# Kernel tuning notes

Measured on AMD Instinct MI355X. Metric: run time of the kernel, lower is better.

## Reference

```python
import jax, jax.numpy as jnp
import numpy as np

N_NODES = 50000
N_EDGES = 1_600_000
F_IN = 128
F_OUT = 8
K_TAPS = 4
AVG_DEG = 32.0


def setup_inputs() -> dict:
    key = jax.random.key(0)
    k1, k2, k3, k4, k5 = jax.random.split(key, 5)
    x = jax.random.normal(k1, (N_NODES, F_IN), dtype=jnp.float32)
    gso_rows = jax.random.randint(k2, (N_EDGES,), 0, N_NODES, dtype=jnp.int32)
    gso_cols = jax.random.randint(k3, (N_EDGES,), 0, N_NODES, dtype=jnp.int32)
    gso_vals = jax.random.uniform(k4, (N_EDGES,), dtype=jnp.float32) / AVG_DEG
    # filterCoeff = randn(outFeat, filter_order) * 0.1 as in torch __init__
    coeff = jax.random.normal(k5, (F_OUT, K_TAPS), dtype=jnp.float32) * 0.1
    return {"x": x, "gso_rows": gso_rows, "gso_cols": gso_cols,
            "gso_vals": gso_vals, "coeff": coeff}


def reference(x, gso_rows, gso_cols, gso_vals, coeff):
    # Faithful to the torch code INCLUDING its carried-over SpMV state:
    # output feature o uses powers S^{1+o(K-1)} .. S^{o(K-1)+K} of x.
    F_out, K = coeff.shape
    N = x.shape[0]
    max_power = F_out * (K - 1) + 1  # highest S power needed

    def spmv(Z):  # S @ Z via edge-list gather + segment_sum scatter
        return jax.ops.segment_sum(gso_vals[:, None] * Z[gso_cols], gso_rows,
                                   num_segments=N)

    def step(Z, _):
        Zn = spmv(Z)
        return Zn, Zn.sum(axis=1)  # sum over in-features done up-front

    # s[p-1, n] = sum_f (S^p x)[n, f], for p = 1..max_power
    _, s = jax.lax.scan(step, x, None, length=max_power)  # (max_power, N)

    # power index (0-based into s) used by output o, tap i: o*(K-1) + i
    idx = jnp.arange(F_out)[:, None] * (K - 1) + jnp.arange(K)[None, :]  # (F_out, K)
    sg = s[idx]  # (F_out, K, N)
    y = jnp.einsum('ok,okn->no', coeff, sg)  # (N, F_out)
    return y
```

## Files before the change

### kernel.cpp

```cpp
#include <hip/hip_runtime.h>
#include <hip/hip_bf16.h>

#define N_NODES 50000
#define N_EDGES 1600000
#define F_IN    128
#define F_OUT   8
#define K_TAPS  4
#define MAX_POWER 25

#define NBLK    256
#define NTHR    512
#define RPB     196
#define CHUNK   4096
#define NPART   391
#define ECAP_G  8192
#define ECAP_L  7168
#define NITER   14
#define CSB     800

#define FSTRIDE 16

__device__ inline int wave_incl_scan(int v, int lane) {
    #pragma unroll
    for (int off = 1; off < 64; off <<= 1) {
        int t = __shfl_up(v, off, 64);
        if (lane >= off) v += t;
    }
    return v;
}

__device__ inline void st_coh(float* p, float v) {
    __hip_atomic_store(p, v, __ATOMIC_RELAXED, __HIP_MEMORY_SCOPE_AGENT);
}
__device__ inline void st_coh_i(int* p, int v) {
    __hip_atomic_store(p, v, __ATOMIC_RELAXED, __HIP_MEMORY_SCOPE_AGENT);
}
__device__ inline int ld_coh_i(const int* p) {
    return __hip_atomic_load((int*)p, __ATOMIC_RELAXED, __HIP_MEMORY_SCOPE_AGENT);
}

__global__ void rowsum_kernel(const float* __restrict__ x,
                              float* __restrict__ u, int n_nodes) {
    int wave_in_block = threadIdx.x >> 6;
    int lane = threadIdx.x & 63;
    int node = blockIdx.x * 4 + wave_in_block;
    if (node >= n_nodes) return;
    const float2* xp = (const float2*)(x + (size_t)node * F_IN);
    float2 v = xp[lane];
    float s = v.x + v.y;
    #pragma unroll
    for (int off = 32; off > 0; off >>= 1)
        s += __shfl_down(s, off, 64);
    if (lane == 0) u[node] = s;
}

__global__ void partition_kernel(const int* __restrict__ rows,
                                 const int* __restrict__ cols,
                                 const float* __restrict__ vals,
                                 int* __restrict__ gcnt,
                                 int2* __restrict__ edges, int n_edges) {
    __shared__ int lhist[NBLK];
    __shared__ int lcur[NBLK];
    __shared__ int lbase[NBLK];
    __shared__ int2 stage[CHUNK];
    __shared__ unsigned char sbkt[CHUNK];
    __shared__ int wsum[4];
    int tid = threadIdx.x;
    int base = blockIdx.x * CHUNK;
    int cend = min(base + CHUNK, n_edges);

    lhist[tid] = 0;
    __syncthreads();
    for (int i = base + tid; i < cend; i += 256)
        atomicAdd(&lhist[rows[i] / RPB], 1);
    __syncthreads();

    int lane = tid & 63, wid = tid >> 6;
    int h = lhist[tid];
    int incl = wave_incl_scan(h, lane);
    if (lane == 63) wsum[wid] = incl;
    __syncthreads();
    int woff = 0;
    for (int w = 0; w < wid; ++w) woff += wsum[w];
    int excl = woff + incl - h;
    lcur[tid] = excl;
    if (h) {
        int g = atomicAdd(&gcnt[tid], h);
        lbase[tid] = tid * ECAP_G + g - excl;
    }
    __syncthreads();

    for (int i = base + tid; i < cend; i += 256) {
        int r = rows[i], c = cols[i];
        float v = vals[i];
        int b = r / RPB;
        int pos = atomicAdd(&lcur[b], 1);
        stage[pos] = make_int2(((r - b * RPB) << 16) | c, __float_as_int(v));
        sbkt[pos] = (unsigned char)b;
    }
    __syncthreads();

    int cn = cend - base;
    for (int i = tid; i < cn; i += 256) {
        int b = sbkt[i];
        int o = lbase[b] + i;
        if (o - b * ECAP_G < ECAP_G)
            edges[o] = stage[i];
    }
}

__global__ __launch_bounds__(NTHR, 1)
void chain_kernel(const int* __restrict__ gcnt,
                  const int2* __restrict__ edges,
                  const float* __restrict__ coeff,
                  const float* __restrict__ u,
                  float* __restrict__ s,
                  float* __restrict__ y,
                  int* __restrict__ flags,
                  int n_nodes) {
    __shared__ int2  esort[ECAP_L];
    __shared__ int   chist[CSB];
    __shared__ int   ccur[CSB];
    __shared__ int   wsum8[8];
    __shared__ float acc[RPB];
    __shared__ float yacc[RPB * F_OUT];
    __shared__ float lcoeff[F_OUT * K_TAPS];

    int tid = threadIdx.x;
    int b = blockIdx.x;

    if (tid < RPB) acc[tid] = 0.f;
    for (int j = tid; j < RPB * F_OUT; j += NTHR) yacc[j] = 0.f;
    if (tid < F_OUT * K_TAPS) lcoeff[tid] = coeff[tid];

    int cnt = min(gcnt[b], ECAP_G);
    const int2* eb = edges + (size_t)b * ECAP_G;

    for (int i = tid; i < CSB; i += NTHR) chist[i] = 0;
    __syncthreads();
    if (cnt <= ECAP_L) {
        for (int i = tid; i < cnt; i += NTHR) {
            int2 e = eb[i];
            atomicAdd(&chist[(e.x & 0xFFFF) >> 6], 1);
        }
        __syncthreads();
        int lane = tid & 63, wid = tid >> 6;
        int b0 = 2 * tid;
        int h0 = (b0 < CSB) ? chist[b0] : 0;
        int h1 = (b0 + 1 < CSB) ? chist[b0 + 1] : 0;
        int ps = h0 + h1;
        int incl = wave_incl_scan(ps, lane);
        if (lane == 63) wsum8[wid] = incl;
        __syncthreads();
        int woff = 0;
        for (int w = 0; w < wid; ++w) woff += wsum8[w];
        int ex = woff + incl - ps;
        if (b0 < CSB) ccur[b0] = ex;
        if (b0 + 1 < CSB) ccur[b0 + 1] = ex + h0;
        __syncthreads();
        for (int i = tid; i < cnt; i += NTHR) {
            int2 e = eb[i];
            int pos = atomicAdd(&ccur[(e.x & 0xFFFF) >> 6], 1);
            esort[pos] = e;
        }
        __syncthreads();
    } else {
        int cl = min(cnt, ECAP_L);
        for (int i = tid; i < cl; i += NTHR) esort[i] = eb[i];
        __syncthreads();
    }

    int   ecol[NITER];
    int   erow[NITER];
    float eval[NITER];
    int cntl = min(cnt, ECAP_L);
    #pragma unroll
    for (int j = 0; j < NITER; ++j) {
        int idx = tid + j * NTHR;
        int2 e = (idx < cntl) ? esort[idx] : make_int2(0, 0);
        ecol[j] = e.x & 0xFFFF;
        erow[j] = e.x >> 16;
        eval[j] = __int_as_float(e.y);
    }

    for (int p = 0; p < MAX_POWER; ++p) {
        const float* __restrict__ src = (p == 0) ? u : s + (size_t)(p - 1) * n_nodes;
        float* dst = s + (size_t)p * n_nodes;

        float v[NITER];
        #pragma unroll
        for (int j = 0; j < NITER; ++j) v[j] = src[ecol[j]];
        #pragma unroll
        for (int j = 0; j < NITER; ++j)
            if (tid + j * NTHR < cntl)
                atomicAdd(&acc[erow[j]], eval[j] * v[j]);
        for (int k = ECAP_L + tid; k < cnt; k += NTHR) {
            int2 ev = eb[k];
            atomicAdd(&acc[ev.x >> 16], __int_as_float(ev.y) * src[ev.x & 0xFFFF]);
        }
        __syncthreads();

        float val = (tid < RPB) ? acc[tid] : 0.f;
        int row = b * RPB + tid;
        bool last = (p == MAX_POWER - 1);
        if (!last && tid < RPB && row < n_nodes) st_coh(&dst[row], val);

        if (!last) {
            __syncthreads();
            if (tid == 0) st_coh_i(&flags[b * FSTRIDE], p + 1);
        }
        if (tid < RPB) {
            acc[tid] = 0.f;
            #pragma unroll
            for (int o = 0; o < F_OUT; ++o) {
                int k = p - (K_TAPS - 1) * o;
                if (k >= 0 && k < K_TAPS)
                    yacc[tid * F_OUT + o] += lcoeff[o * K_TAPS + k] * val;
            }
        }
        if (!last) {
            if (tid < NBLK)
                while (ld_coh_i(&flags[tid * FSTRIDE]) < p + 1)
                    __builtin_amdgcn_s_sleep(2);
            __syncthreads();
        }
    }

    __syncthreads();
    for (int j = tid; j < RPB * F_OUT; j += NTHR) {
        int row = b * RPB + (j >> 3);
        if (row < n_nodes) y[(size_t)row * F_OUT + (j & 7)] = yacc[j];
    }
}

extern "C" void kernel_launch(void* const* d_in, const int* in_sizes, int n_in,
                              void* d_out, int out_size, void* d_ws, size_t ws_size,
                              hipStream_t stream) {
    const float* x        = (const float*)d_in[0];
    const int*   gso_rows = (const int*)d_in[1];
    const int*   gso_cols = (const int*)d_in[2];
    const float* gso_vals = (const float*)d_in[3];
    const float* coeff    = (const float*)d_in[4];
    float* y = (float*)d_out;

    float* u     = (float*)d_ws;
    float* s     = u + N_NODES;
    int2*  edges = (int2*)(s + (size_t)MAX_POWER * N_NODES);
    int*   gcnt  = (int*)(edges + (size_t)NBLK * ECAP_G);
    int*   flags = gcnt + NBLK;

    size_t ctrl_ints = (size_t)NBLK + (size_t)NBLK * FSTRIDE;
    hipMemsetAsync(gcnt, 0, ctrl_ints * sizeof(int), stream);

    partition_kernel<<<NPART, 256, 0, stream>>>(
        gso_rows, gso_cols, gso_vals, gcnt, edges, N_EDGES);

    rowsum_kernel<<<(N_NODES + 3) / 4, 256, 0, stream>>>(x, u, N_NODES);

    int n_nodes = N_NODES;
    void* args[] = { (void*)&gcnt, (void*)&edges, (void*)&coeff,
                     (void*)&u, (void*)&s, (void*)&y, (void*)&flags,
                     (void*)&n_nodes };
    hipLaunchCooperativeKernel((void*)chain_kernel, dim3(NBLK), dim3(NTHR),
                               args, 0, stream);
}
```

Baseline: 419.9 us.

## Pack grid barrier flags densely and vectorize flag polling and row stores

Rewrites the per-power grid barrier. Flags are packed contiguously instead of padded 16 apart, so 64 threads can poll all 256 flags with dwordx4 coherent loads and a wave vote. Each block's 196 row results go out as 49 vectorized coherent stores into a padded stride, followed by a waitcnt before the flag store instead of an extra block barrier. The partition kernel is resized to 256 blocks of 512 threads with larger chunks, and the rowsum kernel handles two nodes per wave with float4 loads. The inline-asm cache bits and the dense flag layout rely on memory-ordering assumptions specific to this hardware.

Result: slower. 475.8 us (+13.3%).

```diff
diff --git a/kernel.cpp b/kernel.cpp
--- a/kernel.cpp
+++ b/kernel.cpp
@@ -2,6 +2,7 @@
 #include <hip/hip_bf16.h>
 
 #define N_NODES 50000
+#define NPAD    50176
 #define N_EDGES 1600000
 #define F_IN    128
 #define F_OUT   8
@@ -11,14 +12,15 @@
 #define NBLK    256
 #define NTHR    512
 #define RPB     196
-#define CHUNK   4096
-#define NPART   391
+#define CHUNK   6272
+#define NPART   256
+#define NTHR_P  512
 #define ECAP_G  8192
 #define ECAP_L  7168
 #define NITER   14
 #define CSB     800
 
-#define FSTRIDE 16
+typedef int v4i __attribute__((ext_vector_type(4)));
 
 __device__ inline int wave_incl_scan(int v, int lane) {
     #pragma unroll
@@ -29,29 +31,36 @@
     return v;
 }
 
-__device__ inline void st_coh(float* p, float v) {
-    __hip_atomic_store(p, v, __ATOMIC_RELAXED, __HIP_MEMORY_SCOPE_AGENT);
-}
 __device__ inline void st_coh_i(int* p, int v) {
     __hip_atomic_store(p, v, __ATOMIC_RELAXED, __HIP_MEMORY_SCOPE_AGENT);
 }
-__device__ inline int ld_coh_i(const int* p) {
-    return __hip_atomic_load((int*)p, __ATOMIC_RELAXED, __HIP_MEMORY_SCOPE_AGENT);
+__device__ inline void st_coh_i4(v4i* p, v4i v) {
+    asm volatile("global_store_dwordx4 %0, %1, off sc0 sc1"
+                 :: "v"(p), "v"(v) : "memory");
+}
+__device__ inline v4i ld_coh_i4(const v4i* p) {
+    v4i v;
+    asm volatile("global_load_dwordx4 %0, %1, off sc0 sc1\n\t"
+                 "s_waitcnt vmcnt(0)"
+                 : "=&v"(v) : "v"(p) : "memory");
+    return v;
 }
 
 __global__ void rowsum_kernel(const float* __restrict__ x,
                               float* __restrict__ u, int n_nodes) {
-    int wave_in_block = threadIdx.x >> 6;
-    int lane = threadIdx.x & 63;
-    int node = blockIdx.x * 4 + wave_in_block;
+    int tid = threadIdx.x;
+    int lane = tid & 63;
+    int wid = tid >> 6;
+    int half = lane >> 5;
+    int l = lane & 31;
+    int node = blockIdx.x * 8 + wid * 2 + half;
     if (node >= n_nodes) return;
-    const float2* xp = (const float2*)(x + (size_t)node * F_IN);
-    float2 v = xp[lane];
-    float s = v.x + v.y;
+    float4 v = ((const float4*)(x + (size_t)node * F_IN))[l];
+    float s = v.x + v.y + v.z + v.w;
     #pragma unroll
-    for (int off = 32; off > 0; off >>= 1)
-        s += __shfl_down(s, off, 64);
-    if (lane == 0) u[node] = s;
+    for (int off = 16; off > 0; off >>= 1)
+        s += __shfl_down(s, off, 32);
+    if (l == 0) u[node] = s;
 }
 
 __global__ void partition_kernel(const int* __restrict__ rows,
@@ -69,28 +78,33 @@
     int base = blockIdx.x * CHUNK;
     int cend = min(base + CHUNK, n_edges);
 
-    lhist[tid] = 0;
-    __syncthreads();
-    for (int i = base + tid; i < cend; i += 256)
+    if (tid < NBLK) lhist[tid] = 0;
+    __syncthreads();
+    for (int i = base + tid; i < cend; i += NTHR_P)
         atomicAdd(&lhist[rows[i] / RPB], 1);
     __syncthreads();
 
     int lane = tid & 63, wid = tid >> 6;
-    int h = lhist[tid];
-    int incl = wave_incl_scan(h, lane);
-    if (lane == 63) wsum[wid] = incl;
-    __syncthreads();
-    int woff = 0;
-    for (int w = 0; w < wid; ++w) woff += wsum[w];
-    int excl = woff + incl - h;
-    lcur[tid] = excl;
-    if (h) {
-        int g = atomicAdd(&gcnt[tid], h);
-        lbase[tid] = tid * ECAP_G + g - excl;
-    }
-    __syncthreads();
-
-    for (int i = base + tid; i < cend; i += 256) {
+    int h = 0, incl = 0;
+    if (tid < NBLK) {
+        h = lhist[tid];
+        incl = wave_incl_scan(h, lane);
+        if (lane == 63) wsum[wid] = incl;
+    }
+    __syncthreads();
+    if (tid < NBLK) {
+        int woff = 0;
+        for (int w = 0; w < wid; ++w) woff += wsum[w];
+        int excl = woff + incl - h;
+        lcur[tid] = excl;
+        if (h) {
+            int g = atomicAdd(&gcnt[tid], h);
+            lbase[tid] = tid * ECAP_G + g - excl;
+        }
+    }
+    __syncthreads();
+
+    for (int i = base + tid; i < cend; i += NTHR_P) {
         int r = rows[i], c = cols[i];
         float v = vals[i];
         int b = r / RPB;
@@ -101,7 +115,7 @@
     __syncthreads();
 
     int cn = cend - base;
-    for (int i = tid; i < cn; i += 256) {
+    for (int i = tid; i < cn; i += NTHR_P) {
         int b = sbkt[i];
         int o = lbase[b] + i;
         if (o - b * ECAP_G < ECAP_G)
@@ -122,7 +136,7 @@
     __shared__ int   chist[CSB];
     __shared__ int   ccur[CSB];
     __shared__ int   wsum8[8];
-    __shared__ float acc[RPB];
+    __shared__ __align__(16) float acc[RPB];
     __shared__ float yacc[RPB * F_OUT];
     __shared__ float lcoeff[F_OUT * K_TAPS];
 
@@ -184,8 +198,8 @@
     }
 
     for (int p = 0; p < MAX_POWER; ++p) {
-        const float* __restrict__ src = (p == 0) ? u : s + (size_t)(p - 1) * n_nodes;
-        float* dst = s + (size_t)p * n_nodes;
+        const float* __restrict__ src = (p == 0) ? u : s + (size_t)(p - 1) * NPAD;
+        float* dst = s + (size_t)p * NPAD;
 
         float v[NITER];
         #pragma unroll
@@ -201,16 +215,14 @@
         __syncthreads();
 
         float val = (tid < RPB) ? acc[tid] : 0.f;
-        int row = b * RPB + tid;
         bool last = (p == MAX_POWER - 1);
-        if (!last && tid < RPB && row < n_nodes) st_coh(&dst[row], val);
-
-        if (!last) {
-            __syncthreads();
-            if (tid == 0) st_coh_i(&flags[b * FSTRIDE], p + 1);
-        }
+
+        if (!last && tid < RPB / 4) {
+            v4i av = ((const v4i*)acc)[tid];
+            st_coh_i4(((v4i*)(dst + (size_t)b * RPB)) + tid, av);
+        }
+
         if (tid < RPB) {
-            acc[tid] = 0.f;
             #pragma unroll
             for (int o = 0; o < F_OUT; ++o) {
                 int k = p - (K_TAPS - 1) * o;
@@ -218,10 +230,24 @@
                     yacc[tid * F_OUT + o] += lcoeff[o * K_TAPS + k] * val;
             }
         }
+
         if (!last) {
-            if (tid < NBLK)
-                while (ld_coh_i(&flags[tid * FSTRIDE]) < p + 1)
-                    __builtin_amdgcn_s_sleep(2);
+            if (tid == 0) {
+                asm volatile("s_waitcnt vmcnt(0)" ::: "memory");
+                st_coh_i(&flags[b], p + 1);
+            }
+            __syncthreads();
+            if (tid < RPB) acc[tid] = 0.f;
+            if (tid < NBLK / 4) {
+                const v4i* fp = ((const v4i*)flags) + tid;
+                int target = p + 1;
+                while (true) {
+                    v4i f = ld_coh_i4(fp);
+                    int m = min(min(f[0], f[1]), min(f[2], f[3]));
+                    if (__all(m >= target)) break;
+                    __builtin_amdgcn_s_sleep(1);
+                }
+            }
             __syncthreads();
         }
     }
@@ -244,23 +270,22 @@
     float* y = (float*)d_out;
 
     float* u     = (float*)d_ws;
-    float* s     = u + N_NODES;
-    int2*  edges = (int2*)(s + (size_t)MAX_POWER * N_NODES);
+    float* s     = u + NPAD;
+    int2*  edges = (int2*)(s + (size_t)MAX_POWER * NPAD);
     int*   gcnt  = (int*)(edges + (size_t)NBLK * ECAP_G);
     int*   flags = gcnt + NBLK;
 
-    size_t ctrl_ints = (size_t)NBLK + (size_t)NBLK * FSTRIDE;
-    hipMemsetAsync(gcnt, 0, ctrl_ints * sizeof(int), stream);
-
-    partition_kernel<<<NPART, 256, 0, stream>>>(
+    (void)hipMemsetAsync(gcnt, 0, (size_t)(NBLK + NBLK) * sizeof(int), stream);
+
+    partition_kernel<<<NPART, NTHR_P, 0, stream>>>(
         gso_rows, gso_cols, gso_vals, gcnt, edges, N_EDGES);
 
-    rowsum_kernel<<<(N_NODES + 3) / 4, 256, 0, stream>>>(x, u, N_NODES);
+    rowsum_kernel<<<(N_NODES + 7) / 8, 256, 0, stream>>>(x, u, N_NODES);
 
     int n_nodes = N_NODES;
     void* args[] = { (void*)&gcnt, (void*)&edges, (void*)&coeff,
                      (void*)&u, (void*)&s, (void*)&y, (void*)&flags,
                      (void*)&n_nodes };
-    hipLaunchCooperativeKernel((void*)chain_kernel, dim3(NBLK), dim3(NTHR),
-                               args, 0, stream);
-}
+    (void)hipLaunchCooperativeKernel((void*)chain_kernel, dim3(NBLK), dim3(NTHR),
+                                     args, 0, stream);
+}
```
